# Performance work log

Hardware: AMD Instinct MI355X
Metric: run time of the kernel (lower is better)

## Reference

```python
import jax, jax.numpy as jnp
import numpy as np

BS, C_REP, H, W = 24, 16, 320, 320
NUM_CLASSES = 4
NUM_MICRO_PROTO = 4
MOMENTUM = 0.99


def setup_inputs() -> dict:
    key = jax.random.key(0)
    k1, k2, k3, k4, k5, k6 = jax.random.split(key, 6)
    rep = jax.random.normal(k1, (BS, C_REP, H, W), dtype=jnp.float32)
    proto_match_idx = jax.random.randint(k2, (BS, H, W, NUM_CLASSES), 0, NUM_MICRO_PROTO, dtype=jnp.int32)
    target = jax.random.randint(k3, (BS, H, W), 0, NUM_CLASSES, dtype=jnp.int32)
    select_mask = jax.random.randint(k4, (H, W), 0, 2, dtype=jnp.int32)
    cond = jax.random.randint(k5, (BS, H, W), 0, 2, dtype=jnp.int32).astype(jnp.bool_)
    protos = jax.random.normal(k6, (NUM_CLASSES, NUM_MICRO_PROTO, C_REP), dtype=jnp.float32)
    return {"rep": rep, "proto_match_idx": proto_match_idx, "target": target,
            "select_mask": select_mask, "cond": cond, "protos": protos}


def reference(rep, proto_match_idx, target, select_mask, cond, protos):
    # Vectorized equivalent of NNet_2d.update_proto:
    #   select pixels where select_mask==1, target!=0, cond True;
    #   group them by (class, micro_proto_idx) where micro_proto_idx is the
    #   column of proto_match_idx chosen by the target class;
    #   take the mean rep per group and EMA-update that prototype.
    bs, c, Hh, Ww = rep.shape
    Ccls, M, _ = protos.shape
    n_seg = Ccls * M

    rep_flat = rep.transpose(0, 2, 3, 1).reshape(-1, c)            # [N, c]
    tgt = target.reshape(-1)                                        # [N]
    pmi = proto_match_idx.reshape(-1, Ccls)                         # [N, Ccls]
    # micro-proto index matched at the target class for each pixel
    pidx = jnp.take_along_axis(pmi, tgt[:, None], axis=-1)[:, 0]    # [N]

    valid = (select_mask[None, :, :] == 1) & (target != 0) & cond   # [bs,H,W]
    w = valid.reshape(-1).astype(rep_flat.dtype)                    # [N]

    seg = tgt * M + pidx                                            # [N] in [0, n_seg)
    sums = jax.ops.segment_sum(rep_flat * w[:, None], seg, num_segments=n_seg)  # [n_seg, c]
    counts = jax.ops.segment_sum(w, seg, num_segments=n_seg)        # [n_seg]

    mean = sums / jnp.maximum(counts, 1.0)[:, None]                 # segment means
    protos_flat = protos.reshape(n_seg, c)
    has_members = (counts > 0)[:, None]
    new_protos = jnp.where(has_members,
                           MOMENTUM * protos_flat + (1.0 - MOMENTUM) * mean,
                           protos_flat)
    return new_protos.reshape(Ccls, M, c)
```

## Files before the change

kernel.cpp:

```cpp
#include <hip/hip_runtime.h>

#define BS 24
#define CREP 16
#define HH 320
#define WW 320
#define HW (HH * WW)
#define TOTAL (BS * HW)
#define NMP 4
#define NSEG 16
#define MOM 0.99f

#define K1_BLOCKS 600
#define TILE 2048
#define NTILES (HW / TILE)
#define NBLK (BS * NTILES)

typedef __attribute__((ext_vector_type(8))) short   bf16x8;
typedef __attribute__((ext_vector_type(4))) float   f32x4;
typedef __attribute__((ext_vector_type(4))) unsigned int u32x4;

__global__ void detect_cond_kernel(const unsigned int* __restrict__ cond_u32,
                                   int* __restrict__ flag) {
    bool big = false;
    for (int i = threadIdx.x; i < 256; i += 64)
        big |= (cond_u32[i] > 1u);
    unsigned long long b = __ballot(big);
    if (threadIdx.x == 0) flag[0] = (b != 0ull) ? 1 : 0;
}

__global__ __launch_bounds__(256) void segmap_kernel(
    const int* __restrict__ pmi,
    const int* __restrict__ tgt,
    const int* __restrict__ smask,
    const unsigned char* __restrict__ cond_b,
    const int* __restrict__ flag,
    unsigned int* __restrict__ segmap32,
    unsigned int* __restrict__ cnt_part)
{
    __shared__ unsigned int hist[NSEG];
    if (threadIdx.x < NSEG) hist[threadIdx.x] = 0u;
    __syncthreads();

    const int byte_layout = flag[0];
    const int4* tgt4  = (const int4*)tgt;
    const int4* cond4 = (const int4*)cond_b;
    const unsigned int* condb = (const unsigned int*)cond_b;

#pragma unroll
    for (int i = 0; i < 4; ++i) {
        const int g = blockIdx.x * 256 + threadIdx.x + i * (K1_BLOCKS * 256);
        const int p = g * 4;
        const int hw = p % HW;
        const int4 t4 = tgt4[g];
        const int4 s4 = *(const int4*)(smask + hw);
        int cc[4];
        if (byte_layout) {
            const unsigned int cb = condb[g];
            cc[0] = cb & 0xff; cc[1] = (cb >> 8) & 0xff;
            cc[2] = (cb >> 16) & 0xff; cc[3] = cb >> 24;
        } else {
            const int4 ci = cond4[g];
            cc[0] = ci.x; cc[1] = ci.y; cc[2] = ci.z; cc[3] = ci.w;
        }
        const int tt[4] = {t4.x, t4.y, t4.z, t4.w};
        const int ss[4] = {s4.x, s4.y, s4.z, s4.w};
        unsigned int packed = 0;
#pragma unroll
        for (int k = 0; k < 4; ++k) {
            int seg = 255;
            if (tt[k] != 0 && ss[k] == 1 && cc[k] != 0) {
                seg = tt[k] * NMP + pmi[(size_t)(p + k) * 4 + tt[k]];
                atomicAdd(&hist[seg], 1u);
            }
            packed |= (unsigned int)(seg & 0xff) << (8 * k);
        }
        segmap32[g] = packed;
    }
    __syncthreads();
    if (threadIdx.x < NSEG)
        cnt_part[(size_t)threadIdx.x * K1_BLOCKS + blockIdx.x] = hist[threadIdx.x];
}

__global__ __launch_bounds__(256) void accum_kernel(
    const float* __restrict__ rep,
    const unsigned char* __restrict__ segmap,
    float* __restrict__ sum_part)
{
    const int b   = blockIdx.x / NTILES;
    const int hw0 = (blockIdx.x % NTILES) * TILE;
    const int tid = threadIdx.x;
    const int l   = tid & 63, wv = tid >> 6;
    const int ch  = l & 15, grp = l >> 4;

    const float* rbase = rep + ((size_t)b * CREP + ch) * HW + hw0 + grp * 8;
    const unsigned char* sbase = segmap + (size_t)b * HW + hw0 + grp * 8;
    const unsigned int chm = (unsigned int)ch;
    const unsigned int one = 0x3F80u;

    f32x4 acc = {0.f, 0.f, 0.f, 0.f};

#pragma unroll 2
    for (int it = wv * 32; it < TILE; it += 128) {
        const float4 v0 = *(const float4*)(rbase + it);
        const float4 v1 = *(const float4*)(rbase + it + 4);
        const unsigned int slo = *(const unsigned int*)(sbase + it);
        const unsigned int shi = *(const unsigned int*)(sbase + it + 4);

        u32x4 au, bu;
        au[0] = (((slo      ) & 0xff) == chm ? one : 0u) |
                (((slo >>  8) & 0xff) == chm ? one << 16 : 0u);
        au[1] = (((slo >> 16) & 0xff) == chm ? one : 0u) |
                (((slo >> 24) & 0xff) == chm ? one << 16 : 0u);
        au[2] = (((shi      ) & 0xff) == chm ? one : 0u) |
                (((shi >>  8) & 0xff) == chm ? one << 16 : 0u);
        au[3] = (((shi >> 16) & 0xff) == chm ? one : 0u) |
                (((shi >> 24) & 0xff) == chm ? one << 16 : 0u);

        bu[0] = (__float_as_uint(v0.x) >> 16) | (__float_as_uint(v0.y) & 0xffff0000u);
        bu[1] = (__float_as_uint(v0.z) >> 16) | (__float_as_uint(v0.w) & 0xffff0000u);
        bu[2] = (__float_as_uint(v1.x) >> 16) | (__float_as_uint(v1.y) & 0xffff0000u);
        bu[3] = (__float_as_uint(v1.z) >> 16) | (__float_as_uint(v1.w) & 0xffff0000u);

        acc = __builtin_amdgcn_mfma_f32_16x16x32_bf16(
            __builtin_bit_cast(bf16x8, au),
            __builtin_bit_cast(bf16x8, bu), acc, 0, 0, 0);
    }

    __shared__ float lacc[4][256];
#pragma unroll
    for (int r = 0; r < 4; ++r)
        lacc[wv][(grp * 4 + r) * 16 + ch] = acc[r];
    __syncthreads();
    if (tid < 256) {
        const float s = lacc[0][tid] + lacc[1][tid] + lacc[2][tid] + lacc[3][tid];
        sum_part[(size_t)tid * NBLK + blockIdx.x] = s;
    }
}

__global__ __launch_bounds__(256) void reduce_kernel(
    const float* __restrict__ sum_part,
    const unsigned int* __restrict__ cnt_part,
    const float* __restrict__ protos,
    float* __restrict__ out)
{
    const int w    = (blockIdx.x * 256 + threadIdx.x) >> 6;
    const int lane = threadIdx.x & 63;
    const int seg  = w >> 4;

    float s = 0.f;
    for (int bb = lane; bb < NBLK; bb += 64)
        s += sum_part[(size_t)w * NBLK + bb];
    int cn = 0;
    for (int bb = lane; bb < K1_BLOCKS; bb += 64)
        cn += (int)cnt_part[(size_t)seg * K1_BLOCKS + bb];
#pragma unroll
    for (int off = 32; off > 0; off >>= 1) {
        s  += __shfl_xor(s, off, 64);
        cn += __shfl_xor(cn, off, 64);
    }
    if (lane == 0) {
        const float cnt  = (float)cn;
        const float mean = s / fmaxf(cnt, 1.0f);
        out[w] = (cn > 0) ? (MOM * protos[w] + (1.0f - MOM) * mean) : protos[w];
    }
}

extern "C" void kernel_launch(void* const* d_in, const int* in_sizes, int n_in,
                              void* d_out, int out_size, void* d_ws, size_t ws_size,
                              hipStream_t stream) {
    const float*         rep    = (const float*)d_in[0];
    const int*           pmi    = (const int*)d_in[1];
    const int*           tgt    = (const int*)d_in[2];
    const int*           smask  = (const int*)d_in[3];
    const unsigned char* cond   = (const unsigned char*)d_in[4];
    const float*         protos = (const float*)d_in[5];
    float*               out    = (float*)d_out;

    unsigned char* ws      = (unsigned char*)d_ws;
    unsigned int* segmap32 = (unsigned int*)ws;
    float*        sum_part = (float*)(ws + (size_t)TOTAL);
    unsigned int* cnt_part = (unsigned int*)(ws + (size_t)TOTAL + 256 * NBLK * 4);
    int*          flag     = (int*)(ws + (size_t)TOTAL + 256 * NBLK * 4 + NSEG * K1_BLOCKS * 4);

    detect_cond_kernel<<<1, 64, 0, stream>>>((const unsigned int*)cond, flag);
    segmap_kernel<<<K1_BLOCKS, 256, 0, stream>>>(pmi, tgt, smask, cond, flag,
                                                 segmap32, cnt_part);
    accum_kernel<<<NBLK, 256, 0, stream>>>(rep, (const unsigned char*)segmap32,
                                           sum_part);
    reduce_kernel<<<64, 256, 0, stream>>>(sum_part, cnt_part, protos, out);
}
```

Measured before the change: 287.3 us.

## Fuse segment-map construction into MFMA accumulation kernel via shared-memory segmap

The separate segmap and accumulation kernels are merged into one kernel per 2048-pixel tile. Each block now builds its packed segment IDs in LDS and consumes them directly, so the global segmap write and read-back and one kernel launch go away. The accumulation loop is also restructured to issue four iterations of rep loads before the MFMAs, giving more memory-level parallelism. Count partials are now indexed per tile block, and the reduce kernel walks the same number of partials for sums and counts. In exchange, each block serializes the label and pmi gather phase before its rep streaming, and there is extra LDS use and register pressure.

Result: faster. 274.1 us (-4.6%).

```diff
diff --git a/kernel.cpp b/kernel.cpp
--- a/kernel.cpp
+++ b/kernel.cpp
@@ -10,7 +10,6 @@
 #define NSEG 16
 #define MOM 0.99f
 
-#define K1_BLOCKS 600
 #define TILE 2048
 #define NTILES (HW / TILE)
 #define NBLK (BS * NTILES)
@@ -28,38 +27,46 @@
     if (threadIdx.x == 0) flag[0] = (b != 0ull) ? 1 : 0;
 }
 
-__global__ __launch_bounds__(256) void segmap_kernel(
+__global__ __launch_bounds__(256) void fused_kernel(
+    const float* __restrict__ rep,
     const int* __restrict__ pmi,
     const int* __restrict__ tgt,
     const int* __restrict__ smask,
     const unsigned char* __restrict__ cond_b,
     const int* __restrict__ flag,
-    unsigned int* __restrict__ segmap32,
+    float* __restrict__ sum_part,
     unsigned int* __restrict__ cnt_part)
 {
+    __shared__ unsigned int segp[TILE / 4];
     __shared__ unsigned int hist[NSEG];
-    if (threadIdx.x < NSEG) hist[threadIdx.x] = 0u;
+    __shared__ float lacc[4][256];
+
+    const int tid = threadIdx.x;
+    if (tid < NSEG) hist[tid] = 0u;
     __syncthreads();
 
+    const int b   = blockIdx.x / NTILES;
+    const int hw0 = (blockIdx.x % NTILES) * TILE;
+    const int p0  = b * HW + hw0;
     const int byte_layout = flag[0];
+
     const int4* tgt4  = (const int4*)tgt;
     const int4* cond4 = (const int4*)cond_b;
     const unsigned int* condb = (const unsigned int*)cond_b;
 
 #pragma unroll
-    for (int i = 0; i < 4; ++i) {
-        const int g = blockIdx.x * 256 + threadIdx.x + i * (K1_BLOCKS * 256);
-        const int p = g * 4;
-        const int hw = p % HW;
-        const int4 t4 = tgt4[g];
-        const int4 s4 = *(const int4*)(smask + hw);
+    for (int j = 0; j < 2; ++j) {
+        const int g  = tid + j * 256;
+        const int gg = (p0 >> 2) + g;
+        const int4 t4 = tgt4[gg];
+        const int4 s4 = *(const int4*)(smask + hw0 + g * 4);
         int cc[4];
         if (byte_layout) {
-            const unsigned int cb = condb[g];
+            const unsigned int cb = condb[gg];
             cc[0] = cb & 0xff; cc[1] = (cb >> 8) & 0xff;
             cc[2] = (cb >> 16) & 0xff; cc[3] = cb >> 24;
         } else {
-            const int4 ci = cond4[g];
+            const int4 ci = cond4[gg];
             cc[0] = ci.x; cc[1] = ci.y; cc[2] = ci.z; cc[3] = ci.w;
         }
         const int tt[4] = {t4.x, t4.y, t4.z, t4.w};
@@ -69,72 +76,68 @@
         for (int k = 0; k < 4; ++k) {
             int seg = 255;
             if (tt[k] != 0 && ss[k] == 1 && cc[k] != 0) {
-                seg = tt[k] * NMP + pmi[(size_t)(p + k) * 4 + tt[k]];
+                seg = tt[k] * NMP + pmi[(size_t)(p0 + g * 4 + k) * 4 + tt[k]];
                 atomicAdd(&hist[seg], 1u);
             }
             packed |= (unsigned int)(seg & 0xff) << (8 * k);
         }
-        segmap32[g] = packed;
+        segp[g] = packed;
     }
     __syncthreads();
-    if (threadIdx.x < NSEG)
-        cnt_part[(size_t)threadIdx.x * K1_BLOCKS + blockIdx.x] = hist[threadIdx.x];
-}
 
-__global__ __launch_bounds__(256) void accum_kernel(
-    const float* __restrict__ rep,
-    const unsigned char* __restrict__ segmap,
-    float* __restrict__ sum_part)
-{
-    const int b   = blockIdx.x / NTILES;
-    const int hw0 = (blockIdx.x % NTILES) * TILE;
-    const int tid = threadIdx.x;
     const int l   = tid & 63, wv = tid >> 6;
     const int ch  = l & 15, grp = l >> 4;
-
     const float* rbase = rep + ((size_t)b * CREP + ch) * HW + hw0 + grp * 8;
-    const unsigned char* sbase = segmap + (size_t)b * HW + hw0 + grp * 8;
+    const unsigned char* sb = (const unsigned char*)segp;
     const unsigned int chm = (unsigned int)ch;
     const unsigned int one = 0x3F80u;
 
     f32x4 acc = {0.f, 0.f, 0.f, 0.f};
 
-#pragma unroll 2
-    for (int it = wv * 32; it < TILE; it += 128) {
-        const float4 v0 = *(const float4*)(rbase + it);
-        const float4 v1 = *(const float4*)(rbase + it + 4);
-        const unsigned int slo = *(const unsigned int*)(sbase + it);
-        const unsigned int shi = *(const unsigned int*)(sbase + it + 4);
+#pragma unroll 1
+    for (int n = 0; n < 4; ++n) {
+        float4 v0[4], v1[4];
+        unsigned int slo[4], shi[4];
+#pragma unroll
+        for (int u = 0; u < 4; ++u) {
+            const int it = wv * 32 + (n * 4 + u) * 128;
+            v0[u] = *(const float4*)(rbase + it);
+            v1[u] = *(const float4*)(rbase + it + 4);
+            slo[u] = *(const unsigned int*)(sb + it + grp * 8);
+            shi[u] = *(const unsigned int*)(sb + it + grp * 8 + 4);
+        }
+#pragma unroll
+        for (int u = 0; u < 4; ++u) {
+            u32x4 au, bu;
+            au[0] = (((slo[u]      ) & 0xff) == chm ? one : 0u) |
+                    (((slo[u] >>  8) & 0xff) == chm ? one << 16 : 0u);
+            au[1] = (((slo[u] >> 16) & 0xff) == chm ? one : 0u) |
+                    (((slo[u] >> 24) & 0xff) == chm ? one << 16 : 0u);
+            au[2] = (((shi[u]      ) & 0xff) == chm ? one : 0u) |
+                    (((shi[u] >>  8) & 0xff) == chm ? one << 16 : 0u);
+            au[3] = (((shi[u] >> 16) & 0xff) == chm ? one : 0u) |
+                    (((shi[u] >> 24) & 0xff) == chm ? one << 16 : 0u);
 
-        u32x4 au, bu;
-        au[0] = (((slo      ) & 0xff) == chm ? one : 0u) |
-                (((slo >>  8) & 0xff) == chm ? one << 16 : 0u);
-        au[1] = (((slo >> 16) & 0xff) == chm ? one : 0u) |
-                (((slo >> 24) & 0xff) == chm ? one << 16 : 0u);
-        au[2] = (((shi      ) & 0xff) == chm ? one : 0u) |
-                (((shi >>  8) & 0xff) == chm ? one << 16 : 0u);
-        au[3] = (((shi >> 16) & 0xff) == chm ? one : 0u) |
-                (((shi >> 24) & 0xff) == chm ? one << 16 : 0u);
+            bu[0] = (__float_as_uint(v0[u].x) >> 16) | (__float_as_uint(v0[u].y) & 0xffff0000u);
+            bu[1] = (__float_as_uint(v0[u].z) >> 16) | (__float_as_uint(v0[u].w) & 0xffff0000u);
+            bu[2] = (__float_as_uint(v1[u].x) >> 16) | (__float_as_uint(v1[u].y) & 0xffff0000u);
+            bu[3] = (__float_as_uint(v1[u].z) >> 16) | (__float_as_uint(v1[u].w) & 0xffff0000u);
 
-        bu[0] = (__float_as_uint(v0.x) >> 16) | (__float_as_uint(v0.y) & 0xffff0000u);
-        bu[1] = (__float_as_uint(v0.z) >> 16) | (__float_as_uint(v0.w) & 0xffff0000u);
-        bu[2] = (__float_as_uint(v1.x) >> 16) | (__float_as_uint(v1.y) & 0xffff0000u);
-        bu[3] = (__float_as_uint(v1.z) >> 16) | (__float_as_uint(v1.w) & 0xffff0000u);
-
-        acc = __builtin_amdgcn_mfma_f32_16x16x32_bf16(
-            __builtin_bit_cast(bf16x8, au),
-            __builtin_bit_cast(bf16x8, bu), acc, 0, 0, 0);
+            acc = __builtin_amdgcn_mfma_f32_16x16x32_bf16(
+                __builtin_bit_cast(bf16x8, au),
+                __builtin_bit_cast(bf16x8, bu), acc, 0, 0, 0);
+        }
     }
 
-    __shared__ float lacc[4][256];
 #pragma unroll
     for (int r = 0; r < 4; ++r)
         lacc[wv][(grp * 4 + r) * 16 + ch] = acc[r];
     __syncthreads();
-    if (tid < 256) {
-        const float s = lacc[0][tid] + lacc[1][tid] + lacc[2][tid] + lacc[3][tid];
-        sum_part[(size_t)tid * NBLK + blockIdx.x] = s;
-    }
+
+    const float s = lacc[0][tid] + lacc[1][tid] + lacc[2][tid] + lacc[3][tid];
+    sum_part[(size_t)tid * NBLK + blockIdx.x] = s;
+    if (tid < NSEG)
+        cnt_part[(size_t)tid * NBLK + blockIdx.x] = hist[tid];
 }
 
 __global__ __launch_bounds__(256) void reduce_kernel(
@@ -148,11 +151,11 @@
     const int seg  = w >> 4;
 
     float s = 0.f;
-    for (int bb = lane; bb < NBLK; bb += 64)
-        s += sum_part[(size_t)w * NBLK + bb];
     int cn = 0;
-    for (int bb = lane; bb < K1_BLOCKS; bb += 64)
-        cn += (int)cnt_part[(size_t)seg * K1_BLOCKS + bb];
+    for (int bb = lane; bb < NBLK; bb += 64) {
+        s  += sum_part[(size_t)w * NBLK + bb];
+        cn += (int)cnt_part[(size_t)seg * NBLK + bb];
+    }
 #pragma unroll
     for (int off = 32; off > 0; off >>= 1) {
         s  += __shfl_xor(s, off, 64);
@@ -177,15 +180,12 @@
     float*               out    = (float*)d_out;
 
     unsigned char* ws      = (unsigned char*)d_ws;
-    unsigned int* segmap32 = (unsigned int*)ws;
-    float*        sum_part = (float*)(ws + (size_t)TOTAL);
-    unsigned int* cnt_part = (unsigned int*)(ws + (size_t)TOTAL + 256 * NBLK * 4);
-    int*          flag     = (int*)(ws + (size_t)TOTAL + 256 * NBLK * 4 + NSEG * K1_BLOCKS * 4);
+    float*        sum_part = (float*)ws;
+    unsigned int* cnt_part = (unsigned int*)(ws + (size_t)256 * NBLK * 4);
+    int*          flag     = (int*)(ws + (size_t)256 * NBLK * 4 + (size_t)NSEG * NBLK * 4);
 
     detect_cond_kernel<<<1, 64, 0, stream>>>((const unsigned int*)cond, flag);
-    segmap_kernel<<<K1_BLOCKS, 256, 0, stream>>>(pmi, tgt, smask, cond, flag,
-                                                 segmap32, cnt_part);
-    accum_kernel<<<NBLK, 256, 0, stream>>>(rep, (const unsigned char*)segmap32,
-                                           sum_part);
+    fused_kernel<<<NBLK, 256, 0, stream>>>(rep, pmi, tgt, smask, cond, flag,
+                                           sum_part, cnt_part);
     reduce_kernel<<<64, 256, 0, stream>>>(sum_part, cnt_part, protos, out);
 }
```
